# Optimization experiments

Measured on AMD Instinct MI355X. Metric: run time of the kernel, lower is better.

Reference implementation:

```python
import jax, jax.numpy as jnp
import numpy as np
import math

HIDDEN = 1024
N_HEADS = 16
HEAD = HIDDEN // N_HEADS

def setup_inputs() -> dict:
    key = jax.random.key(0)
    k1, k2, k3 = jax.random.split(key, 3)
    encodings = jax.random.normal(k1, (2, 2048, HIDDEN), dtype=jnp.float32)
    W_attn = jax.random.normal(k2, (HIDDEN, 3 * HIDDEN), dtype=jnp.float32) * 0.02
    b_attn = jnp.zeros((3 * HIDDEN,), dtype=jnp.float32)
    W_out = jax.random.normal(k3, (HIDDEN, HIDDEN), dtype=jnp.float32) * 0.02
    b_out = jnp.zeros((HIDDEN,), dtype=jnp.float32)
    return {"encodings": encodings, "W_attn": W_attn, "b_attn": b_attn,
            "W_out": W_out, "b_out": b_out}

def reference(encodings, W_attn, b_attn, W_out, b_out):
    b, n, _ = encodings.shape
    qkv = encodings @ W_attn + b_attn              # [b, n, 3*hidden]
    q, k, v = jnp.split(qkv, 3, axis=-1)
    # 'b n (h l) -> b h n l'
    def to_heads(t):
        return t.reshape(b, n, N_HEADS, HEAD).transpose(0, 2, 1, 3)
    q, k, v = to_heads(q), to_heads(k), to_heads(v)
    # scores[b,h,k,q]; causal mask keeps key_pos <= query_pos
    scores = jnp.einsum('bhki,bhqi->bhkq', k, q) / math.sqrt(HEAD)
    mask = jnp.arange(n)[:, None] <= jnp.arange(n)[None, :]   # [k, q]
    scores = jnp.where(mask, scores, jnp.float32(-10000.0))
    attn = jax.nn.softmax(scores, axis=2)          # softmax over key dim
    combined = jnp.einsum('bhkq,bhkl->bhql', attn, v)  # [b, h, n, head]
    out = combined.transpose(0, 2, 1, 3).reshape(b, n, HIDDEN)
    return out @ W_out + b_out
```

## Files before the change

kernel.cpp:

```cpp
#include <hip/hip_runtime.h>
#include <hip/hip_bf16.h>

typedef __attribute__((ext_vector_type(8))) short bf16x8;
typedef __attribute__((ext_vector_type(4))) short bf16x4;
typedef __attribute__((ext_vector_type(4))) float f32x4;

__device__ __forceinline__ short f2bf(float f) {
    unsigned u = __float_as_uint(f);
    u += 0x7fff + ((u >> 16) & 1);
    return (short)(u >> 16);
}
__device__ __forceinline__ float bf2f(short s) {
    return __uint_as_float(((unsigned)(unsigned short)s) << 16);
}
__device__ __forceinline__ unsigned pk_bf16(float lo, float hi) {
    __hip_bfloat162 t = __float22bfloat162_rn(make_float2(lo, hi));
    unsigned u;
    __builtin_memcpy(&u, &t, 4);
    return u;
}

#define GLOAD_LDS16(gp, lp)                                                            \
    __builtin_amdgcn_global_load_lds(                                                  \
        (const __attribute__((address_space(1))) unsigned*)(gp),                       \
        (__attribute__((address_space(3))) unsigned*)(lp), 16, 0, 0)

#define QK_SCALE 0.180336879f
#define MFMA16(a, b, c) __builtin_amdgcn_mfma_f32_16x16x32_bf16((a), (b), (c), 0, 0, 0)

__device__ __forceinline__ void tcvt_tile(const float* __restrict__ W, short* __restrict__ Wt,
                                          int K, int N, int bx, int by, int t,
                                          short (*tile)[72]) {
    const int k0 = by * 64, n0 = bx * 64;
    #pragma unroll
    for (int jj = 0; jj < 4; ++jj) {
        int row = jj * 16 + (t >> 4);
        int col = (t & 15) * 4;
        f32x4 v = *(const f32x4*)&W[(size_t)(k0 + row) * N + n0 + col];
        bf16x4 b = {f2bf(v.x), f2bf(v.y), f2bf(v.z), f2bf(v.w)};
        *(bf16x4*)&tile[row][col] = b;
    }
    __syncthreads();
    const int nr = t >> 2, kc = (t & 3) * 16;
    bf16x8 o0, o1;
    #pragma unroll
    for (int j = 0; j < 8; ++j) { o0[j] = tile[kc + j][nr]; o1[j] = tile[kc + 8 + j][nr]; }
    short* dst = &Wt[(size_t)(n0 + nr) * K + k0 + kc];
    *(bf16x8*)dst = o0;
    *(bf16x8*)(dst + 8) = o1;
}

__global__ __launch_bounds__(256) void prep_kernel(
    const float* __restrict__ enc, const float* __restrict__ Wa,
    const float* __restrict__ ba, const float* __restrict__ Wo,
    const float* __restrict__ bo, short* __restrict__ Abf,
    short* __restrict__ WtA, short* __restrict__ bbA,
    short* __restrict__ WtO, short* __restrict__ bbO)
{
    __shared__ alignas(16) short tile[64][72];
    const int id = blockIdx.x, t = threadIdx.x;
    if (id < 2048) {
        const int i = id * 2048 + t * 8;
        f32x4 a = *(const f32x4*)&enc[i];
        f32x4 b = *(const f32x4*)&enc[i + 4];
        bf16x8 o = {f2bf(a.x), f2bf(a.y), f2bf(a.z), f2bf(a.w),
                    f2bf(b.x), f2bf(b.y), f2bf(b.z), f2bf(b.w)};
        *(bf16x8*)&Abf[i] = o;
    } else if (id == 2048) {
        for (int j = t * 8; j < 3072; j += 2048) {
            f32x4 a = *(const f32x4*)&ba[j];
            f32x4 b = *(const f32x4*)&ba[j + 4];
            bf16x8 o = {f2bf(a.x), f2bf(a.y), f2bf(a.z), f2bf(a.w),
                        f2bf(b.x), f2bf(b.y), f2bf(b.z), f2bf(b.w)};
            *(bf16x8*)&bbA[j] = o;
        }
    } else if (id == 2049) {
        if (t < 128) {
            const int j = t * 8;
            f32x4 a = *(const f32x4*)&bo[j];
            f32x4 b = *(const f32x4*)&bo[j + 4];
            bf16x8 o = {f2bf(a.x), f2bf(a.y), f2bf(a.z), f2bf(a.w),
                        f2bf(b.x), f2bf(b.y), f2bf(b.z), f2bf(b.w)};
            *(bf16x8*)&bbO[j] = o;
        }
        __syncthreads();
    } else if (id < 2818) {
        const int lid = id - 2050;
        tcvt_tile(Wa, WtA, 1024, 3072, lid % 48, lid / 48, t, tile);
    } else {
        const int lid = id - 2818;
        tcvt_tile(Wo, WtO, 1024, 1024, lid % 16, lid / 16, t, tile);
    }
}

template<int BN, bool F32OUT, bool SPLIT3>
__global__ __launch_bounds__(256) void gemm_bt(
    const short* __restrict__ A, const short* __restrict__ Bt,
    const short* __restrict__ bias, void* __restrict__ C,
    short* __restrict__ Kw, short* __restrict__ Vw, int M, int N, int K)
{
    __shared__ alignas(16) short As[128 * 32];
    __shared__ alignas(16) short Bs[BN * 32];

    const int tid = threadIdx.x, w = tid >> 6, lane = tid & 63;
    const int quad = lane >> 4, l16 = lane & 15;
    constexpr int MT = (BN == 128) ? 4 : 2;
    const int wm = (BN == 128) ? (w >> 1) : w;
    const int wn = (BN == 128) ? (w & 1) : 0;
    const int m0 = blockIdx.y * 128, n0 = blockIdx.x * BN;
    const int srow = lane >> 2, scol = (lane & 3) * 8;

    f32x4 acc[MT][4] = {};

    for (int k0 = 0; k0 < K; k0 += 32) {
        __syncthreads();
        #pragma unroll
        for (int jj = 0; jj < 2; ++jj) {
            const int rb = w * 32 + jj * 16;
            GLOAD_LDS16(&A[(size_t)(m0 + rb + srow) * K + k0 + scol], &As[rb * 32]);
        }
        if (BN == 128) {
            #pragma unroll
            for (int jj = 0; jj < 2; ++jj) {
                const int rb = w * 32 + jj * 16;
                GLOAD_LDS16(&Bt[(size_t)(n0 + rb + srow) * K + k0 + scol], &Bs[rb * 32]);
            }
        } else {
            const int rb = w * 16;
            GLOAD_LDS16(&Bt[(size_t)(n0 + rb + srow) * K + k0 + scol], &Bs[rb * 32]);
        }
        __syncthreads();
        bf16x8 af[MT], bfr[4];
        #pragma unroll
        for (int i = 0; i < MT; ++i)
            af[i] = *(const bf16x8*)&As[(wm * (MT * 16) + i * 16 + l16) * 32 + quad * 8];
        #pragma unroll
        for (int i = 0; i < 4; ++i)
            bfr[i] = *(const bf16x8*)&Bs[(wn * 64 + i * 16 + l16) * 32 + quad * 8];
        #pragma unroll
        for (int mt = 0; mt < MT; ++mt)
            #pragma unroll
            for (int nt = 0; nt < 4; ++nt)
                acc[mt][nt] = MFMA16(af[mt], bfr[nt], acc[mt][nt]);
    }

    if (SPLIT3) {
        const int g = n0 >> 10;
        short* dstb = (g == 0) ? (short*)C : (g == 1) ? Kw : Vw;
        const int lc0 = n0 & 1023;
        #pragma unroll
        for (int nt = 0; nt < 4; ++nt) {
            const int col = n0 + wn * 64 + nt * 16 + l16;
            const int lc = lc0 + wn * 64 + nt * 16 + l16;
            const float bv = bf2f(bias[col]);
            #pragma unroll
            for (int mt = 0; mt < 4; ++mt) {
                const int row = m0 + wm * 64 + mt * 16 + quad * 4;
                #pragma unroll
                for (int r = 0; r < 4; ++r) {
                    float v = acc[mt][nt][r] + bv;
                    if (g == 0) v *= QK_SCALE;
                    dstb[(size_t)(row + r) * 1024 + lc] = f2bf(v);
                }
            }
        }
    } else {
        #pragma unroll
        for (int nt = 0; nt < 4; ++nt) {
            const int col = n0 + wn * 64 + nt * 16 + l16;
            const float bv = bf2f(bias[col]);
            #pragma unroll
            for (int mt = 0; mt < MT; ++mt) {
                const int row = m0 + wm * (MT * 16) + mt * 16 + quad * 4;
                #pragma unroll
                for (int r = 0; r < 4; ++r) {
                    float v = acc[mt][nt][r] + bv;
                    if (F32OUT) ((float*)C)[(size_t)(row + r) * N + col] = v;
                    else        ((short*)C)[(size_t)(row + r) * N + col] = f2bf(v);
                }
            }
        }
    }
}

__global__ __launch_bounds__(256) void fragprep_kernel(
    const short* __restrict__ Kw, const short* __restrict__ Vw,
    short* __restrict__ Kx, short* __restrict__ Vx)
{
    __shared__ alignas(16) short T[64][72];
    const int t = threadIdx.x;
    const int kc = blockIdx.x, bh = blockIdx.y;
    const int batch = bh >> 4, head = bh & 15;
    const size_t srcbase = ((size_t)batch * 2048 + kc * 64) * 1024 + head * 64;
    short* kxdst = Kx + ((size_t)bh * 32 + kc) * 4096;
    short* vxdst = Vx + ((size_t)bh * 32 + kc) * 4096;

    #pragma unroll
    for (int i = 0; i < 2; ++i) {
        const int c = i * 256 + t;
        const int lane = c & 63, sh = c >> 6;
        const int s = sh >> 1, h = sh & 1;
        const int l16 = lane & 15, quad = lane >> 4;
        bf16x8 v = *(const bf16x8*)&Kw[srcbase + (size_t)(s * 16 + l16) * 1024 + h * 32 + quad * 8];
        *(bf16x8*)&kxdst[c * 8] = v;
    }
    #pragma unroll
    for (int i = 0; i < 2; ++i) {
        const int c = i * 256 + t;
        const int row = c >> 3, d0 = (c & 7) * 8;
        bf16x8 v = *(const bf16x8*)&Vw[srcbase + (size_t)row * 1024 + d0];
        #pragma unroll
        for (int j = 0; j < 8; ++j) T[d0 + j][row] = v[j];
    }
    __syncthreads();
    #pragma unroll
    for (int i = 0; i < 2; ++i) {
        const int c = i * 256 + t;
        const int lane = c & 63, hd = c >> 6;
        const int h = hd >> 2, dt = hd & 3;
        const int l16 = lane & 15, quad = lane >> 4;
        bf16x8 v = *(const bf16x8*)&T[dt * 16 + l16][h * 32 + quad * 8];
        *(bf16x8*)&vxdst[c * 8] = v;
    }
}

__global__ __launch_bounds__(256) void attn_kernel(
    const short* __restrict__ Qw, const short* __restrict__ Kx,
    const short* __restrict__ Vx, short* __restrict__ comb)
{
    __shared__ alignas(16) short Ps[4][2][16 * 72];
    __shared__ alignas(16) float cbuf[2][2][64][16];
    __shared__ float clacc[2][2][64];

    const int tid = threadIdx.x, w4 = tid >> 6, lane = tid & 63;
    const int w = w4 & 1;
    const int h = w4 >> 1;
    const int quad = lane >> 4, l16 = lane & 15;
    const int bh = blockIdx.x;
    const int tA = blockIdx.y, tB = 63 - tA;
    const int batch = bh >> 4, head = bh & 15;
    const size_t rowbase = (size_t)batch * 2048;
    const int hcol = head * 64;
    const int q0A = tA * 32 + w * 16, q0B = tB * 32 + w * 16;
    const int diagA = tA >> 1, diagB = tB >> 1;
    const short* Kxbh = Kx + (size_t)bh * 131072;
    const short* Vxbh = Vx + (size_t)bh * 131072;
    const int lofs = lane * 8;
    short* pwA = &Ps[w4][0][0];
    short* pwB = &Ps[w4][1][0];

    bf16x8 qfA[2], qfB[2];
    {
        const short* pa = &Qw[(rowbase + q0A + l16) * 1024 + hcol];
        const short* pb = &Qw[(rowbase + q0B + l16) * 1024 + hcol];
        qfA[0] = *(const bf16x8*)(pa + quad * 8);
        qfA[1] = *(const bf16x8*)(pa + 32 + quad * 8);
        qfB[0] = *(const bf16x8*)(pb + quad * 8);
        qfB[1] = *(const bf16x8*)(pb + 32 + quad * 8);
    }

    f32x4 otA[4] = {}, otB[4] = {};
    float laccA = 0.f, laccB = 0.f;

    bf16x8 kf[4][2];
    {
        const short* kb0 = Kxbh + (size_t)h * 4096;
        #pragma unroll
        for (int s = 0; s < 4; ++s) {
            kf[s][0] = *(const bf16x8*)&kb0[(s * 2 + 0) * 512 + lofs];
            kf[s][1] = *(const bf16x8*)&kb0[(s * 2 + 1) * 512 + lofs];
        }
    }

    for (int kc = h; kc <= diagB; kc += 2) {
        const bool actA = (kc <= diagA);
        const int key0 = kc * 64;

        const short* vb = Vxbh + (size_t)kc * 4096;
        bf16x8 vf[2][4];
        #pragma unroll
        for (int hh = 0; hh < 2; ++hh)
            #pragma unroll
            for (int dt = 0; dt < 4; ++dt)
                vf[hh][dt] = *(const bf16x8*)&vb[(hh * 4 + dt) * 512 + lofs];

        f32x4 svA[4], svB[4];
        #pragma unroll
        for (int s = 0; s < 4; ++s) {
            f32x4 a = {0.f, 0.f, 0.f, 0.f};
            a = MFMA16(kf[s][0], qfB[0], a);
            a = MFMA16(kf[s][1], qfB[1], a);
            svB[s] = a;
            if (actA) {
                f32x4 b = {0.f, 0.f, 0.f, 0.f};
                b = MFMA16(kf[s][0], qfA[0], b);
                b = MFMA16(kf[s][1], qfA[1], b);
                svA[s] = b;
            }
        }

        if (kc + 2 <= diagB) {
            const short* kb = Kxbh + (size_t)(kc + 2) * 4096;
            #pragma unroll
            for (int s = 0; s < 4; ++s) {
                kf[s][0] = *(const bf16x8*)&kb[(s * 2 + 0) * 512 + lofs];
                kf[s][1] = *(const bf16x8*)&kb[(s * 2 + 1) * 512 + lofs];
            }
        }

        if (kc == diagB) {
            const int qq = q0B + l16;
            #pragma unroll
            for (int s = 0; s < 4; ++s) {
                const int keyb = key0 + s * 16 + quad * 4;
                #pragma unroll
                for (int r = 0; r < 4; ++r)
                    svB[s][r] = (keyb + r <= qq) ? svB[s][r] : -1e30f;
            }
        }
        #pragma unroll
        for (int s = 0; s < 4; ++s) {
            #pragma unroll
            for (int r = 0; r < 4; ++r) svB[s][r] = exp2f(svB[s][r]);
            laccB += (svB[s][0] + svB[s][1]) + (svB[s][2] + svB[s][3]);
            *(unsigned*)&pwB[l16 * 72 + s * 16 + quad * 4]     = pk_bf16(svB[s][0], svB[s][1]);
            *(unsigned*)&pwB[l16 * 72 + s * 16 + quad * 4 + 2] = pk_bf16(svB[s][2], svB[s][3]);
        }
        if (actA) {
            if (kc == diagA) {
                const int qq = q0A + l16;
                #pragma unroll
                for (int s = 0; s < 4; ++s) {
                    const int keyb = key0 + s * 16 + quad * 4;
                    #pragma unroll
                    for (int r = 0; r < 4; ++r)
                        svA[s][r] = (keyb + r <= qq) ? svA[s][r] : -1e30f;
                }
            }
            #pragma unroll
            for (int s = 0; s < 4; ++s) {
                #pragma unroll
                for (int r = 0; r < 4; ++r) svA[s][r] = exp2f(svA[s][r]);
                laccA += (svA[s][0] + svA[s][1]) + (svA[s][2] + svA[s][3]);
                *(unsigned*)&pwA[l16 * 72 + s * 16 + quad * 4]     = pk_bf16(svA[s][0], svA[s][1]);
                *(unsigned*)&pwA[l16 * 72 + s * 16 + quad * 4 + 2] = pk_bf16(svA[s][2], svA[s][3]);
            }
        }

        {
            bf16x8 pfB0 = *(const bf16x8*)&pwB[l16 * 72 + quad * 8];
            bf16x8 pfB1 = *(const bf16x8*)&pwB[l16 * 72 + 32 + quad * 8];
            #pragma unroll
            for (int dt = 0; dt < 4; ++dt) {
                otB[dt] = MFMA16(vf[0][dt], pfB0, otB[dt]);
                otB[dt] = MFMA16(vf[1][dt], pfB1, otB[dt]);
            }
            if (actA) {
                bf16x8 pfA0 = *(const bf16x8*)&pwA[l16 * 72 + quad * 8];
                bf16x8 pfA1 = *(const bf16x8*)&pwA[l16 * 72 + 32 + quad * 8];
                #pragma unroll
                for (int dt = 0; dt < 4; ++dt) {
                    otA[dt] = MFMA16(vf[0][dt], pfA0, otA[dt]);
                    otA[dt] = MFMA16(vf[1][dt], pfA1, otA[dt]);
                }
            }
        }
    }

    __syncthreads();
    if (h == 1) {
        #pragma unroll
        for (int dt = 0; dt < 4; ++dt) {
            *(f32x4*)&cbuf[w][0][lane][dt * 4] = otA[dt];
            *(f32x4*)&cbuf[w][1][lane][dt * 4] = otB[dt];
        }
        clacc[w][0][lane] = laccA;
        clacc[w][1][lane] = laccB;
    }
    __syncthreads();
    if (h == 0) {
        #pragma unroll
        for (int dt = 0; dt < 4; ++dt) {
            otA[dt] += *(const f32x4*)&cbuf[w][0][lane][dt * 4];
            otB[dt] += *(const f32x4*)&cbuf[w][1][lane][dt * 4];
        }
        laccA += clacc[w][0][lane];
        laccB += clacc[w][1][lane];

        laccA += __shfl_xor(laccA, 16);
        laccA += __shfl_xor(laccA, 32);
        laccB += __shfl_xor(laccB, 16);
        laccB += __shfl_xor(laccB, 32);
        const float invA = 1.0f / laccA, invB = 1.0f / laccB;

        #pragma unroll
        for (int dt = 0; dt < 4; ++dt) {
            *(unsigned*)&pwA[l16 * 72 + dt * 16 + quad * 4]     = pk_bf16(otA[dt][0] * invA, otA[dt][1] * invA);
            *(unsigned*)&pwA[l16 * 72 + dt * 16 + quad * 4 + 2] = pk_bf16(otA[dt][2] * invA, otA[dt][3] * invA);
            *(unsigned*)&pwB[l16 * 72 + dt * 16 + quad * 4]     = pk_bf16(otB[dt][0] * invB, otB[dt][1] * invB);
            *(unsigned*)&pwB[l16 * 72 + dt * 16 + quad * 4 + 2] = pk_bf16(otB[dt][2] * invB, otB[dt][3] * invB);
        }
        {
            const int qr = lane >> 2, dc = (lane & 3) * 16;
            bf16x8 a0 = *(const bf16x8*)&pwA[qr * 72 + dc];
            bf16x8 a1 = *(const bf16x8*)&pwA[qr * 72 + dc + 8];
            short* dstA = &comb[(rowbase + q0A + qr) * 1024 + hcol + dc];
            *(bf16x8*)dstA = a0;
            *(bf16x8*)(dstA + 8) = a1;
            bf16x8 b0 = *(const bf16x8*)&pwB[qr * 72 + dc];
            bf16x8 b1 = *(const bf16x8*)&pwB[qr * 72 + dc + 8];
            short* dstB = &comb[(rowbase + q0B + qr) * 1024 + hcol + dc];
            *(bf16x8*)dstB = b0;
            *(bf16x8*)(dstB + 8) = b1;
        }
    }
}

extern "C" void kernel_launch(void* const* d_in, const int* in_sizes, int n_in,
                              void* d_out, int out_size, void* d_ws, size_t ws_size,
                              hipStream_t stream)
{
    const float* enc = (const float*)d_in[0];
    const float* Wa  = (const float*)d_in[1];
    const float* ba  = (const float*)d_in[2];
    const float* Wo  = (const float*)d_in[3];
    const float* bo  = (const float*)d_in[4];
    float* out = (float*)d_out;

    char* ws = (char*)d_ws;
    short* Abf  = (short*)ws;
    short* Kx   = (short*)ws;
    short* WtO  = (short*)(ws + ((size_t)8 << 20));
    short* bbA  = (short*)(ws + ((size_t)10 << 20));
    short* bbO  = (short*)(ws + ((size_t)10 << 20) + 16384);
    short* WtA  = (short*)(ws + ((size_t)11 << 20));
    short* Vx   = (short*)(ws + ((size_t)11 << 20));
    short* Qw   = (short*)(ws + ((size_t)19 << 20));
    short* Kw   = (short*)(ws + ((size_t)27 << 20));
    short* comb = (short*)(ws + ((size_t)27 << 20));
    short* Vw   = (short*)(ws + ((size_t)35 << 20));

    prep_kernel<<<3074, 256, 0, stream>>>(enc, Wa, ba, Wo, bo, Abf, WtA, bbA, WtO, bbO);
    gemm_bt<128, false, true><<<dim3(24, 32), 256, 0, stream>>>(
        Abf, WtA, bbA, Qw, Kw, Vw, 4096, 3072, 1024);
    fragprep_kernel<<<dim3(32, 32), 256, 0, stream>>>(Kw, Vw, Kx, Vx);
    attn_kernel<<<dim3(32, 32), 256, 0, stream>>>(Qw, Kx, Vx, comb);
    gemm_bt<64, true, false><<<dim3(16, 32), 256, 0, stream>>>(
        comb, WtO, bbO, out, nullptr, nullptr, 4096, 1024, 1024);
}
```

Measured before the change: 194.7 us.

## Fuse K/V fragment prep into QKV GEMM epilogue via swizzled LDS staging

The QKV GEMM epilogue now stages each 128x128 output tile in XOR-swizzled shared memory, then writes Q row-major and K/V straight into the MFMA-fragment layouts the attention kernel reads. This removes the separate fragprep kernel launch and its extra global round trip of K and V, and turns scattered 2-byte stores into 16-byte vector stores. In exchange it adds a 32KB LDS buffer to the GEMM, which may lower occupancy, plus a barrier, and the workspace is remapped.

```diff
diff --git a/kernel.cpp b/kernel.cpp
--- a/kernel.cpp
+++ b/kernel.cpp
@@ -101,6 +101,7 @@
 {
     __shared__ alignas(16) short As[128 * 32];
     __shared__ alignas(16) short Bs[BN * 32];
+    __shared__ alignas(16) short Ct[SPLIT3 ? 128 * 128 : 1];
 
     const int tid = threadIdx.x, w = tid >> 6, lane = tid & 63;
     const int quad = lane >> 4, l16 = lane & 15;
@@ -146,22 +147,80 @@
 
     if (SPLIT3) {
         const int g = n0 >> 10;
-        short* dstb = (g == 0) ? (short*)C : (g == 1) ? Kw : Vw;
         const int lc0 = n0 & 1023;
-        #pragma unroll
-        for (int nt = 0; nt < 4; ++nt) {
-            const int col = n0 + wn * 64 + nt * 16 + l16;
-            const int lc = lc0 + wn * 64 + nt * 16 + l16;
-            const float bv = bf2f(bias[col]);
-            #pragma unroll
-            for (int mt = 0; mt < 4; ++mt) {
-                const int row = m0 + wm * 64 + mt * 16 + quad * 4;
-                #pragma unroll
-                for (int r = 0; r < 4; ++r) {
-                    float v = acc[mt][nt][r] + bv;
-                    if (g == 0) v *= QK_SCALE;
-                    dstb[(size_t)(row + r) * 1024 + lc] = f2bf(v);
+        if (g < 2) {
+            #pragma unroll
+            for (int nt = 0; nt < 4; ++nt) {
+                const int col = wn * 64 + nt * 16 + l16;
+                const float bv = bf2f(bias[n0 + col]);
+                const int chunk = col >> 3, wi = col & 7;
+                #pragma unroll
+                for (int mt = 0; mt < 4; ++mt) {
+                    const int rbase = wm * 64 + mt * 16 + quad * 4;
+                    #pragma unroll
+                    for (int r = 0; r < 4; ++r) {
+                        const int row = rbase + r;
+                        float v = acc[mt][nt][r] + bv;
+                        if (g == 0) v *= QK_SCALE;
+                        Ct[row * 128 + (((chunk ^ (row & 15)) << 3) | wi)] = f2bf(v);
+                    }
                 }
+            }
+        } else {
+            #pragma unroll
+            for (int nt = 0; nt < 4; ++nt) {
+                const int d = wn * 64 + nt * 16 + l16;
+                const float bv = bf2f(bias[n0 + d]);
+                const int dsw = d & 15;
+                #pragma unroll
+                for (int mt = 0; mt < 4; ++mt) {
+                    const int key0 = wm * 64 + mt * 16 + quad * 4;
+                    bf16x4 p = {f2bf(acc[mt][nt][0] + bv), f2bf(acc[mt][nt][1] + bv),
+                                f2bf(acc[mt][nt][2] + bv), f2bf(acc[mt][nt][3] + bv)};
+                    *(bf16x4*)&Ct[d * 128 + ((((key0 >> 3) ^ dsw) << 3) | (key0 & 7))] = p;
+                }
+            }
+        }
+        __syncthreads();
+        const int batch = m0 >> 11;
+        const int kc0 = (m0 & 2047) >> 6;
+        const int head0 = lc0 >> 6;
+        if (g == 0) {
+            short* dst = (short*)C;
+            #pragma unroll
+            for (int i = 0; i < 8; ++i) {
+                const int idx = i * 256 + tid;
+                const int row = idx >> 4, chunk = idx & 15;
+                bf16x8 v = *(const bf16x8*)&Ct[row * 128 + ((chunk ^ (row & 15)) << 3)];
+                *(bf16x8*)&dst[(size_t)(m0 + row) * 1024 + lc0 + chunk * 8] = v;
+            }
+        } else if (g == 1) {
+            #pragma unroll
+            for (int i = 0; i < 8; ++i) {
+                const int idx = i * 256 + tid;
+                const int qd = idx >> 9, c = idx & 511;
+                const int kcL = qd >> 1, headL = qd & 1;
+                const int s = c >> 7, h2 = (c >> 6) & 1;
+                const int l16c = c & 15, quadc = (c >> 4) & 3;
+                const int row = kcL * 64 + s * 16 + l16c;
+                const int colc = headL * 8 + h2 * 4 + quadc;
+                bf16x8 v = *(const bf16x8*)&Ct[row * 128 + ((colc ^ (row & 15)) << 3)];
+                const int bh = batch * 16 + head0 + headL, kc = kc0 + kcL;
+                *(bf16x8*)&Kw[((size_t)(bh * 32 + kc) * 512 + c) * 8] = v;
+            }
+        } else {
+            #pragma unroll
+            for (int i = 0; i < 8; ++i) {
+                const int idx = i * 256 + tid;
+                const int qd = idx >> 9, c = idx & 511;
+                const int kcL = qd >> 1, headL = qd & 1;
+                const int h2 = c >> 8, dt = (c >> 6) & 3;
+                const int l16c = c & 15, quadc = (c >> 4) & 3;
+                const int d = headL * 64 + dt * 16 + l16c;
+                const int keyc = kcL * 8 + h2 * 4 + quadc;
+                bf16x8 v = *(const bf16x8*)&Ct[d * 128 + ((keyc ^ (d & 15)) << 3)];
+                const int bh = batch * 16 + head0 + headL, kc = kc0 + kcL;
+                *(bf16x8*)&Vw[((size_t)(bh * 32 + kc) * 512 + c) * 8] = v;
             }
         }
     } else {
@@ -180,47 +239,6 @@
                 }
             }
         }
-    }
-}
-
-__global__ __launch_bounds__(256) void fragprep_kernel(
-    const short* __restrict__ Kw, const short* __restrict__ Vw,
-    short* __restrict__ Kx, short* __restrict__ Vx)
-{
-    __shared__ alignas(16) short T[64][72];
-    const int t = threadIdx.x;
-    const int kc = blockIdx.x, bh = blockIdx.y;
-    const int batch = bh >> 4, head = bh & 15;
-    const size_t srcbase = ((size_t)batch * 2048 + kc * 64) * 1024 + head * 64;
-    short* kxdst = Kx + ((size_t)bh * 32 + kc) * 4096;
-    short* vxdst = Vx + ((size_t)bh * 32 + kc) * 4096;
-
-    #pragma unroll
-    for (int i = 0; i < 2; ++i) {
-        const int c = i * 256 + t;
-        const int lane = c & 63, sh = c >> 6;
-        const int s = sh >> 1, h = sh & 1;
-        const int l16 = lane & 15, quad = lane >> 4;
-        bf16x8 v = *(const bf16x8*)&Kw[srcbase + (size_t)(s * 16 + l16) * 1024 + h * 32 + quad * 8];
-        *(bf16x8*)&kxdst[c * 8] = v;
-    }
-    #pragma unroll
-    for (int i = 0; i < 2; ++i) {
-        const int c = i * 256 + t;
-        const int row = c >> 3, d0 = (c & 7) * 8;
-        bf16x8 v = *(const bf16x8*)&Vw[srcbase + (size_t)row * 1024 + d0];
-        #pragma unroll
-        for (int j = 0; j < 8; ++j) T[d0 + j][row] = v[j];
-    }
-    __syncthreads();
-    #pragma unroll
-    for (int i = 0; i < 2; ++i) {
-        const int c = i * 256 + t;
-        const int lane = c & 63, hd = c >> 6;
-        const int h = hd >> 2, dt = hd & 3;
-        const int l16 = lane & 15, quad = lane >> 4;
-        bf16x8 v = *(const bf16x8*)&T[dt * 16 + l16][h * 32 + quad * 8];
-        *(bf16x8*)&vxdst[c * 8] = v;
     }
 }
 
@@ -429,21 +447,18 @@
 
     char* ws = (char*)d_ws;
     short* Abf  = (short*)ws;
-    short* Kx   = (short*)ws;
+    short* comb = (short*)ws;
     short* WtO  = (short*)(ws + ((size_t)8 << 20));
     short* bbA  = (short*)(ws + ((size_t)10 << 20));
     short* bbO  = (short*)(ws + ((size_t)10 << 20) + 16384);
     short* WtA  = (short*)(ws + ((size_t)11 << 20));
-    short* Vx   = (short*)(ws + ((size_t)11 << 20));
-    short* Qw   = (short*)(ws + ((size_t)19 << 20));
-    short* Kw   = (short*)(ws + ((size_t)27 << 20));
-    short* comb = (short*)(ws + ((size_t)27 << 20));
-    short* Vw   = (short*)(ws + ((size_t)35 << 20));
+    short* Kx   = (short*)(ws + ((size_t)17 << 20));
+    short* Vx   = (short*)(ws + ((size_t)25 << 20));
+    short* Qw   = (short*)(ws + ((size_t)33 << 20));
 
     prep_kernel<<<3074, 256, 0, stream>>>(enc, Wa, ba, Wo, bo, Abf, WtA, bbA, WtO, bbO);
     gemm_bt<128, false, true><<<dim3(24, 32), 256, 0, stream>>>(
-        Abf, WtA, bbA, Qw, Kw, Vw, 4096, 3072, 1024);
-    fragprep_kernel<<<dim3(32, 32), 256, 0, stream>>>(Kw, Vw, Kx, Vx);
+        Abf, WtA, bbA, Qw, Kx, Vx, 4096, 3072, 1024);
     attn_kernel<<<dim3(32, 32), 256, 0, stream>>>(Qw, Kx, Vx, comb);
     gemm_bt<64, true, false><<<dim3(16, 32), 256, 0, stream>>>(
         comb, WtO, bbO, out, nullptr, nullptr, 4096, 1024, 1024);
```

New measurement: 201.6 us. +3.5%, slower.
